# Kernel optimization log

Hardware: AMD Instinct MI355X
Metric: run time of the kernel (lower is better)

The kernel has to match this reference:

```python
import jax, jax.numpy as jnp
import numpy as np


def setup_inputs() -> dict:
    key = jax.random.key(0)
    k1, k2, k3 = jax.random.split(key, 3)
    B, E, N, D = 64, 4096, 512, 128
    messages = jax.random.normal(k1, (B, E, D), dtype=jnp.float32)
    tgt_indices = jax.random.randint(k2, (B, E), 0, N, dtype=jnp.int32)
    atom_features_ref = jax.random.normal(k3, (B, N, D), dtype=jnp.float32)
    return {"messages": messages, "tgt_indices": tgt_indices,
            "atom_features_ref": atom_features_ref}


def reference(messages, tgt_indices, atom_features_ref):
    # messages: [B, E, D], tgt_indices: [B, E] in [0, N), atom_features_ref: [B, N, D']
    B, E, D = messages.shape
    N = atom_features_ref.shape[1]
    # Flatten batch into segment ids: segment = b * N + tgt_index
    offset = jnp.arange(B, dtype=tgt_indices.dtype)[:, None] * N   # [B, 1]
    flat_idx = (tgt_indices + offset).reshape(-1)                   # [B*E]
    flat_msgs = messages.reshape(-1, D)                             # [B*E, D]
    aggregated = jax.ops.segment_sum(flat_msgs, flat_idx, num_segments=B * N)
    return aggregated.reshape(B, N, D)
```

## Files before the change

kernel.cpp:

```cpp
#include <hip/hip_runtime.h>

constexpr int B = 64, E = 4096, N = 512, D = 128;
constexpr int QN = 64;
constexpr int THREADS = 512;
constexpr int EPT = E / THREADS;
constexpr int NBLK = B * (N / QN);

__global__ __launch_bounds__(THREADS)
void fused_seg_sum(const float* __restrict__ msgs,
                   const int* __restrict__ tgt,
                   float* __restrict__ out) {
    __shared__ int cnt[QN];
    __shared__ int loff[QN + 1];
    __shared__ unsigned short lst[E];

    const int tid  = threadIdx.x;
    const int lane = tid & 63;
    const int w    = tid >> 6;
    const int b    = blockIdx.x >> 3;
    const int n0   = (blockIdx.x & 7) * QN;

    if (tid < QN) cnt[tid] = 0;
    __syncthreads();

    const int* tb = tgt + b * E;
    int tn[EPT];
    #pragma unroll
    for (int t = 0; t < EPT; ++t) {
        tn[t] = tb[t * THREADS + tid] - n0;
        if ((unsigned)tn[t] < (unsigned)QN) atomicAdd(&cnt[tn[t]], 1);
    }
    __syncthreads();

    if (w == 0) {
        const int c = cnt[lane];
        int x = c;
        #pragma unroll
        for (int d = 1; d < 64; d <<= 1) {
            const int y = __shfl_up(x, d);
            if (lane >= d) x += y;
        }
        const int excl = x - c;
        loff[lane] = excl;
        cnt[lane]  = excl;
        if (lane == 63) loff[QN] = x;
    }
    __syncthreads();

    #pragma unroll
    for (int t = 0; t < EPT; ++t) {
        if ((unsigned)tn[t] < (unsigned)QN) {
            const int pos = atomicAdd(&cnt[tn[t]], 1);
            lst[pos] = (unsigned short)(t * THREADS + tid);
        }
    }
    __syncthreads();

    const float2* mb = reinterpret_cast<const float2*>(msgs) + (size_t)b * E * 64;
    float2* ob = reinterpret_cast<float2*>(out) + ((size_t)b * N + n0) * 64;
    #pragma unroll
    for (int s = 0; s < 8; ++s) {
        const int n    = w * 8 + s;
        const int base = loff[n];
        const int k    = loff[n + 1] - base;
        float ax = 0.f, ay = 0.f;
        for (int i = 0; i < k; i += 8) {
            int ee[8]; float wt[8];
            #pragma unroll
            for (int j = 0; j < 8; ++j) {
                const bool v = (i + j < k);
                ee[j] = v ? (int)lst[base + i + j] : 0;
                wt[j] = v ? 1.f : 0.f;
            }
            float2 vv[8];
            #pragma unroll
            for (int j = 0; j < 8; ++j)
                vv[j] = mb[(size_t)ee[j] * 64 + lane];
            #pragma unroll
            for (int j = 0; j < 8; ++j) { ax += wt[j] * vv[j].x; ay += wt[j] * vv[j].y; }
        }
        float2 r; r.x = ax; r.y = ay;
        ob[(size_t)n * 64 + lane] = r;
    }
}

extern "C" void kernel_launch(void* const* d_in, const int* in_sizes, int n_in,
                              void* d_out, int out_size, void* d_ws, size_t ws_size,
                              hipStream_t stream) {
    const float* msgs = (const float*)d_in[0];
    const int*   tgt  = (const int*)d_in[1];
    float* out = (float*)d_out;
    fused_seg_sum<<<NBLK, THREADS, 0, stream>>>(msgs, tgt, out);
}
```

Baseline: 33.02 us.

## Gather float4 rows with half-wave edge split and paired segment processing

```diff
diff --git a/kernel.cpp b/kernel.cpp
--- a/kernel.cpp
+++ b/kernel.cpp
@@ -40,9 +40,8 @@
             const int y = __shfl_up(x, d);
             if (lane >= d) x += y;
         }
-        const int excl = x - c;
-        loff[lane] = excl;
-        cnt[lane]  = excl;
+        loff[lane] = x - c;
+        cnt[lane]  = x - c;
         if (lane == 63) loff[QN] = x;
     }
     __syncthreads();
@@ -56,31 +55,65 @@
     }
     __syncthreads();
 
-    const float2* mb = reinterpret_cast<const float2*>(msgs) + (size_t)b * E * 64;
-    float2* ob = reinterpret_cast<float2*>(out) + ((size_t)b * N + n0) * 64;
+    const float4* mb4 = reinterpret_cast<const float4*>(msgs) + (size_t)b * E * 32;
+    float4*       ob4 = reinterpret_cast<float4*>(out) + ((size_t)b * N + n0) * 32;
+    const int half = lane >> 5;
+    const int l32  = lane & 31;
+
     #pragma unroll
-    for (int s = 0; s < 8; ++s) {
-        const int n    = w * 8 + s;
-        const int base = loff[n];
-        const int k    = loff[n + 1] - base;
-        float ax = 0.f, ay = 0.f;
-        for (int i = 0; i < k; i += 8) {
-            int ee[8]; float wt[8];
+    for (int sp = 0; sp < 4; ++sp) {
+        const int nA = w * 8 + sp;
+        const int nB = nA + 4;
+        const int baseA = loff[nA]; const int kA = loff[nA + 1] - baseA;
+        const int baseB = loff[nB]; const int kB = loff[nB + 1] - baseB;
+        float4 accA = {0.f, 0.f, 0.f, 0.f};
+        float4 accB = {0.f, 0.f, 0.f, 0.f};
+        const int pmax = (max(kA, kB) + 1) >> 1;
+
+        for (int p0 = 0; p0 < pmax; p0 += 4) {
+            float4 vA[4], vB[4];
             #pragma unroll
-            for (int j = 0; j < 8; ++j) {
-                const bool v = (i + j < k);
-                ee[j] = v ? (int)lst[base + i + j] : 0;
-                wt[j] = v ? 1.f : 0.f;
+            for (int j = 0; j < 4; ++j) {
+                const int p = p0 + j;
+                if (2 * p < kA) {
+                    const int e0 = lst[baseA + 2 * p];
+                    const int e1 = (2 * p + 1 < kA) ? (int)lst[baseA + 2 * p + 1] : 0;
+                    const int e  = half ? e1 : e0;
+                    vA[j] = mb4[(size_t)e * 32 + l32];
+                }
+                if (2 * p < kB) {
+                    const int e0 = lst[baseB + 2 * p];
+                    const int e1 = (2 * p + 1 < kB) ? (int)lst[baseB + 2 * p + 1] : 0;
+                    const int e  = half ? e1 : e0;
+                    vB[j] = mb4[(size_t)e * 32 + l32];
+                }
             }
-            float2 vv[8];
             #pragma unroll
-            for (int j = 0; j < 8; ++j)
-                vv[j] = mb[(size_t)ee[j] * 64 + lane];
-            #pragma unroll
-            for (int j = 0; j < 8; ++j) { ax += wt[j] * vv[j].x; ay += wt[j] * vv[j].y; }
+            for (int j = 0; j < 4; ++j) {
+                const int p = p0 + j;
+                if (2 * p < kA) {
+                    const float wa = (!half || (2 * p + 1 < kA)) ? 1.f : 0.f;
+                    accA.x += wa * vA[j].x; accA.y += wa * vA[j].y;
+                    accA.z += wa * vA[j].z; accA.w += wa * vA[j].w;
+                }
+                if (2 * p < kB) {
+                    const float wb = (!half || (2 * p + 1 < kB)) ? 1.f : 0.f;
+                    accB.x += wb * vB[j].x; accB.y += wb * vB[j].y;
+                    accB.z += wb * vB[j].z; accB.w += wb * vB[j].w;
+                }
+            }
         }
-        float2 r; r.x = ax; r.y = ay;
-        ob[(size_t)n * 64 + lane] = r;
+
+        accA.x += __shfl(accA.x, lane ^ 32); accA.y += __shfl(accA.y, lane ^ 32);
+        accA.z += __shfl(accA.z, lane ^ 32); accA.w += __shfl(accA.w, lane ^ 32);
+        accB.x += __shfl(accB.x, lane ^ 32); accB.y += __shfl(accB.y, lane ^ 32);
+        accB.z += __shfl(accB.z, lane ^ 32); accB.w += __shfl(accB.w, lane ^ 32);
+
+        float4 st;
+        st.x = half ? accB.x : accA.x; st.y = half ? accB.y : accA.y;
+        st.z = half ? accB.z : accA.z; st.w = half ? accB.w : accA.w;
+        const int ns = half ? nB : nA;
+        ob4[(size_t)ns * 32 + l32] = st;
     }
 }
 
```

Result: slower. 35.60 us (+7.8%).
